# Kernel optimization log

Hardware: AMD Instinct MI355X
Metric: run time of the kernel (lower is better)

Reference implementation:

```python
import jax, jax.numpy as jnp
import numpy as np

TAU = 0.5
EPS = 1e-12  # torch F.normalize default eps


def _l2norm(x):
    n = jnp.sqrt(jnp.sum(x * x, axis=1, keepdims=True))
    return x / jnp.maximum(n, EPS)


def _semi_loss(z1, z2, tau):
    z1n = _l2norm(z1)
    z2n = _l2norm(z2)
    refl = jnp.exp(jnp.matmul(z1n, z1n.T) / tau)      # [N, N]
    between = jnp.exp(jnp.matmul(z1n, z2n.T) / tau)   # [N, N]
    num = jnp.diagonal(between)
    den = refl.sum(axis=1) + between.sum(axis=1) - jnp.diagonal(refl)
    return -jnp.mean(jnp.log(num / den))


def setup_inputs() -> dict:
    key = jax.random.key(0)
    k1, k2 = jax.random.split(key)
    N, D = 8192, 256
    H_1 = jax.random.normal(k1, (N, D), dtype=jnp.float32)
    H_2 = jax.random.normal(k2, (N, D), dtype=jnp.float32)
    return {"H_1": H_1, "H_2": H_2}


def reference(H_1, H_2):
    l1 = _semi_loss(H_1, H_2, TAU)
    l2 = _semi_loss(H_2, H_1, TAU)
    return (l1 + l2) * 0.5
```

## Files before the change

kernel.cpp:

```cpp
#include <hip/hip_runtime.h>
#include <hip/hip_bf16.h>
#include <math.h>

#define NROW 8192
#define DDIM 256
#define BM 128
#define BN 128
#define BK 128
#define NT_SYM 2080
#define NT_FULL 4096

typedef __attribute__((ext_vector_type(4))) float f32x4;
typedef __attribute__((address_space(3))) unsigned int lds_u32;
typedef const __attribute__((address_space(1))) unsigned int glb_u32;

template <int CTRL>
static __device__ inline float dpp_ror_add(float v) {
    int s = __float_as_int(v);
    int r = __builtin_amdgcn_update_dpp(0, s, CTRL, 0xF, 0xF, true);
    return v + __int_as_float(r);
}
static __device__ inline float row16_sum(float v) {
    v = dpp_ror_add<0x121>(v);
    v = dpp_ror_add<0x122>(v);
    v = dpp_ror_add<0x124>(v);
    v = dpp_ror_add<0x128>(v);
    return v;
}

static __device__ inline unsigned int pack_fp8x4(float a, float b, float c, float d) {
    int p = __builtin_amdgcn_cvt_pk_fp8_f32(a, b, 0, false);
    p = __builtin_amdgcn_cvt_pk_fp8_f32(c, d, p, true);
    return (unsigned int)p;
}

__global__ __launch_bounds__(256) void normalize_kernel(
        const float* __restrict__ h1, const float* __restrict__ h2,
        unsigned char* __restrict__ z1b, unsigned char* __restrict__ z2b,
        float* __restrict__ diag,
        float* __restrict__ rs1, float* __restrict__ rs2,
        float* __restrict__ rbr, float* __restrict__ rbc,
        float* __restrict__ out) {
    int wave = threadIdx.x >> 6;
    int lane = threadIdx.x & 63;
    int row  = blockIdx.x * 4 + wave;
    if (blockIdx.x == 0 && threadIdx.x == 0) out[0] = 0.f;
    const float4* p1 = (const float4*)(h1 + (size_t)row * DDIM);
    const float4* p2 = (const float4*)(h2 + (size_t)row * DDIM);
    float4 a = p1[lane];
    float4 b = p2[lane];
    float s1 = a.x*a.x + a.y*a.y + a.z*a.z + a.w*a.w;
    float s2 = b.x*b.x + b.y*b.y + b.z*b.z + b.w*b.w;
    #pragma unroll
    for (int m = 1; m < 64; m <<= 1) { s1 += __shfl_xor(s1, m); s2 += __shfl_xor(s2, m); }
    float r1 = 1.0f / fmaxf(sqrtf(s1), 1e-12f);
    float r2 = 1.0f / fmaxf(sqrtf(s2), 1e-12f);
    float n1x = a.x*r1, n1y = a.y*r1, n1z = a.z*r1, n1w = a.w*r1;
    float n2x = b.x*r2, n2y = b.y*r2, n2z = b.z*r2, n2w = b.w*r2;
    float dt = n1x*n2x + n1y*n2y + n1z*n2z + n1w*n2w;
    #pragma unroll
    for (int m = 1; m < 64; m <<= 1) dt += __shfl_xor(dt, m);
    if (lane == 0) {
        diag[row] = 2.0f * dt;
        rs1[row] = 0.f; rs2[row] = 0.f; rbr[row] = 0.f; rbc[row] = 0.f;
    }
    const float SC = 1.69864364f;
    ((unsigned int*)(z1b + (size_t)row * DDIM))[lane] =
        pack_fp8x4(n1x*SC, n1y*SC, n1z*SC, n1w*SC);
    ((unsigned int*)(z2b + (size_t)row * DDIM))[lane] =
        pack_fp8x4(n2x*SC, n2y*SC, n2z*SC, n2w*SC);
}

__global__ __launch_bounds__(256, 4) void expsum_kernel(
        const unsigned char* __restrict__ z1, const unsigned char* __restrict__ z2,
        float* __restrict__ rs1, float* __restrict__ rs2,
        float* __restrict__ rbr, float* __restrict__ rbc) {
    int b = blockIdx.x;
    int kind, t;
    if (b < NT_SYM)            { kind = 0; t = b; }
    else if (b < 2 * NT_SYM)   { kind = 1; t = b - NT_SYM; }
    else                       { kind = 2; t = b - 2 * NT_SYM; }

    int by, bx;
    const unsigned char *Ap, *Bp;
    float *rowsum, *colsum;
    if (kind == 2) {
        by = t >> 6; bx = t & 63;
        Ap = z1; Bp = z2; rowsum = rbr; colsum = rbc;
    } else {
        by = (int)((sqrtf(8.0f * (float)t + 1.0f) - 1.0f) * 0.5f);
        while ((by + 1) * (by + 2) / 2 <= t) ++by;
        while (by * (by + 1) / 2 > t) --by;
        bx = t - by * (by + 1) / 2;
        const unsigned char* z = (kind == 0) ? z1 : z2;
        Ap = z; Bp = z;
        rowsum = (kind == 0) ? rs1 : rs2;
        colsum = (bx == by) ? nullptr : rowsum;
    }

    const int rt = by * BM;
    const int ct = bx * BN;

    __shared__ __align__(16) unsigned char lA[BM * BK];
    __shared__ __align__(16) unsigned char lB[BN * BK];

    const int tid  = threadIdx.x;
    const int lane = tid & 63;
    const int wid  = tid >> 6;
    const int wr   = wid >> 1;
    const int wc   = wid & 1;
    const int quad = lane >> 4;
    const int l15  = lane & 15;

    const int srow = lane >> 3;
    const int sgt  = lane & 7;

    f32x4 acc[4][4];
    #pragma unroll
    for (int mi = 0; mi < 4; ++mi)
        #pragma unroll
        for (int ni = 0; ni < 4; ++ni)
            acc[mi][ni] = (f32x4){0.f, 0.f, 0.f, 0.f};

    for (int kt = 0; kt < DDIM; kt += BK) {
        #pragma unroll
        for (int p = 0; p < 4; ++p) {
            int r0 = (p * 4 + wid) * 8;
            int r  = r0 + srow;
            int gg = sgt ^ ((r >> 1) & 7);
            const unsigned char* ga = Ap + (size_t)(rt + r) * DDIM + kt + gg * 16;
            __builtin_amdgcn_global_load_lds((glb_u32*)ga, (lds_u32*)(lA + r0 * BK), 16, 0, 0);
            const unsigned char* gb = Bp + (size_t)(ct + r) * DDIM + kt + gg * 16;
            __builtin_amdgcn_global_load_lds((glb_u32*)gb, (lds_u32*)(lB + r0 * BK), 16, 0, 0);
        }
        __syncthreads();
        #pragma unroll
        for (int ks = 0; ks < 4; ++ks) {
            long af[4], bfr[4];
            const int g    = ks * 2 + (quad >> 1);
            const int half = (quad & 1) * 8;
            #pragma unroll
            for (int mi = 0; mi < 4; ++mi) {
                int r = wr * 64 + mi * 16 + l15;
                int phys = (g ^ ((r >> 1) & 7)) * 16 + half;
                af[mi] = *((const long*)(lA + r * BK + phys));
            }
            #pragma unroll
            for (int ni = 0; ni < 4; ++ni) {
                int c = wc * 64 + ni * 16 + l15;
                int phys = (g ^ ((c >> 1) & 7)) * 16 + half;
                bfr[ni] = *((const long*)(lB + c * BK + phys));
            }
            #pragma unroll
            for (int mi = 0; mi < 4; ++mi)
                #pragma unroll
                for (int ni = 0; ni < 4; ++ni)
                    acc[mi][ni] = __builtin_amdgcn_mfma_f32_16x16x32_fp8_fp8(
                        af[mi], bfr[ni], acc[mi][ni], 0, 0, 0);
        }
        __syncthreads();
    }

    float colpart[4] = {0.f, 0.f, 0.f, 0.f};
    #pragma unroll
    for (int mi = 0; mi < 4; ++mi) {
        #pragma unroll
        for (int r = 0; r < 4; ++r) {
            float rp = 0.f;
            #pragma unroll
            for (int ni = 0; ni < 4; ++ni) {
                float e = exp2f(acc[mi][ni][r]);
                rp += e;
                colpart[ni] += e;
            }
            rp = row16_sum(rp);
            if (l15 == 0) {
                int grow = rt + wr * 64 + mi * 16 + quad * 4 + r;
                atomicAdd(&rowsum[grow], rp);
            }
        }
    }
    if (colsum) {
        #pragma unroll
        for (int ni = 0; ni < 4; ++ni) {
            float cp = colpart[ni];
            cp += __shfl_xor(cp, 16);
            cp += __shfl_xor(cp, 32);
            if (lane < 16) {
                int gcol = ct + wc * 64 + ni * 16 + l15;
                atomicAdd(&colsum[gcol], cp);
            }
        }
    }
}

__global__ __launch_bounds__(256) void finalize_kernel(
        const float* __restrict__ rs1, const float* __restrict__ rs2,
        const float* __restrict__ rbr, const float* __restrict__ rbc,
        const float* __restrict__ diag, float* __restrict__ out) {
    __shared__ float s4[4];
    const float E2 = 7.38905609893065f;
    int i = blockIdx.x * 256 + threadIdx.x;
    float den1 = rs1[i] + rbr[i] - E2;
    float den2 = rs2[i] + rbc[i] - E2;
    float v = 0.5f * (logf(den1) + logf(den2)) - diag[i];
    #pragma unroll
    for (int m = 1; m < 64; m <<= 1) v += __shfl_xor(v, m);
    if ((threadIdx.x & 63) == 0) s4[threadIdx.x >> 6] = v;
    __syncthreads();
    if (threadIdx.x == 0) {
        float t = (s4[0] + s4[1] + s4[2] + s4[3]) * (1.0f / (float)NROW);
        atomicAdd(out, t);
    }
}

extern "C" void kernel_launch(void* const* d_in, const int* in_sizes, int n_in,
                              void* d_out, int out_size, void* d_ws, size_t ws_size,
                              hipStream_t stream) {
    const float* h1 = (const float*)d_in[0];
    const float* h2 = (const float*)d_in[1];
    float* out = (float*)d_out;

    char* ws = (char*)d_ws;
    unsigned char* z1b = (unsigned char*)ws;
    unsigned char* z2b = (unsigned char*)(ws + (size_t)NROW * DDIM);
    float* sums = (float*)(ws + (size_t)2 * NROW * DDIM);
    float* rs1  = sums;
    float* rs2  = sums + NROW;
    float* rbr  = sums + 2 * NROW;
    float* rbc  = sums + 3 * NROW;
    float* diag = sums + 4 * NROW;

    normalize_kernel<<<NROW / 4, 256, 0, stream>>>(h1, h2, z1b, z2b, diag,
                                                   rs1, rs2, rbr, rbc, out);

    expsum_kernel<<<2 * NT_SYM + NT_FULL, 256, 0, stream>>>(z1b, z2b, rs1, rs2, rbr, rbc);

    finalize_kernel<<<NROW / 256, 256, 0, stream>>>(rs1, rs2, rbr, rbc, diag, out);
}
```

Before: 169.1 us.

## Use 16x16x128 scaled FP8 MFMA with reworked LDS swizzle and wider fragment loads

Replaces four K-steps of the 16x16x32 FP8 MFMA with one gfx950 scaled MFMA (16x16x128 f8f6f4) per tile pair, using unity scales (0x7F). Operand fragments are now loaded as two 16-byte LDS reads per lane instead of 8-byte reads, and the swizzle is changed from (r>>1)&7 to r&7 to match the new access pattern. This is meant to cut MFMA issue count and LDS instruction count in the inner loop. The larger i32x8 fragments raise register pressure, so launch bounds drop from 4 to 3 blocks per CU, and correctness depends on the lane-to-K mapping matching the new instruction's operand layout.

```diff
diff --git a/kernel.cpp b/kernel.cpp
--- a/kernel.cpp
+++ b/kernel.cpp
@@ -11,6 +11,8 @@
 #define NT_FULL 4096
 
 typedef __attribute__((ext_vector_type(4))) float f32x4;
+typedef __attribute__((ext_vector_type(4))) int   i32x4;
+typedef __attribute__((ext_vector_type(8))) int   i32x8;
 typedef __attribute__((address_space(3))) unsigned int lds_u32;
 typedef const __attribute__((address_space(1))) unsigned int glb_u32;
 
@@ -71,7 +73,7 @@
         pack_fp8x4(n2x*SC, n2y*SC, n2z*SC, n2w*SC);
 }
 
-__global__ __launch_bounds__(256, 4) void expsum_kernel(
+__global__ __launch_bounds__(256, 3) void expsum_kernel(
         const unsigned char* __restrict__ z1, const unsigned char* __restrict__ z2,
         float* __restrict__ rs1, float* __restrict__ rs2,
         float* __restrict__ rbr, float* __restrict__ rbc) {
@@ -114,6 +116,13 @@
 
     const int srow = lane >> 3;
     const int sgt  = lane & 7;
+    const int gg   = sgt ^ srow;
+
+    const int s7 = l15 & 7;
+    const unsigned char* aLo = lA + (wr * 64 + l15) * BK + (((quad << 1)    ) ^ s7) * 16;
+    const unsigned char* aHi = lA + (wr * 64 + l15) * BK + (((quad << 1) | 1) ^ s7) * 16;
+    const unsigned char* bLo = lB + (wc * 64 + l15) * BK + (((quad << 1)    ) ^ s7) * 16;
+    const unsigned char* bHi = lB + (wc * 64 + l15) * BK + (((quad << 1) | 1) ^ s7) * 16;
 
     f32x4 acc[4][4];
     #pragma unroll
@@ -126,38 +135,35 @@
         #pragma unroll
         for (int p = 0; p < 4; ++p) {
             int r0 = (p * 4 + wid) * 8;
-            int r  = r0 + srow;
-            int gg = sgt ^ ((r >> 1) & 7);
-            const unsigned char* ga = Ap + (size_t)(rt + r) * DDIM + kt + gg * 16;
+            const unsigned char* ga = Ap + (size_t)(rt + r0 + srow) * DDIM + kt + gg * 16;
             __builtin_amdgcn_global_load_lds((glb_u32*)ga, (lds_u32*)(lA + r0 * BK), 16, 0, 0);
-            const unsigned char* gb = Bp + (size_t)(ct + r) * DDIM + kt + gg * 16;
+            const unsigned char* gb = Bp + (size_t)(ct + r0 + srow) * DDIM + kt + gg * 16;
             __builtin_amdgcn_global_load_lds((glb_u32*)gb, (lds_u32*)(lB + r0 * BK), 16, 0, 0);
         }
         __syncthreads();
-        #pragma unroll
-        for (int ks = 0; ks < 4; ++ks) {
-            long af[4], bfr[4];
-            const int g    = ks * 2 + (quad >> 1);
-            const int half = (quad & 1) * 8;
+
+        i32x8 af[4], bfr[4];
+        #pragma unroll
+        for (int mi = 0; mi < 4; ++mi) {
+            i32x4 lo = *((const i32x4*)(aLo + mi * 16 * BK));
+            i32x4 hi = *((const i32x4*)(aHi + mi * 16 * BK));
+            af[mi] = __builtin_shufflevector(lo, hi, 0, 1, 2, 3, 4, 5, 6, 7);
+        }
+        #pragma unroll
+        for (int ni = 0; ni < 4; ++ni) {
+            i32x4 lo = *((const i32x4*)(bLo + ni * 16 * BK));
+            i32x4 hi = *((const i32x4*)(bHi + ni * 16 * BK));
+            bfr[ni] = __builtin_shufflevector(lo, hi, 0, 1, 2, 3, 4, 5, 6, 7);
+        }
+        #pragma unroll
+        for (int mi = 0; mi < 4; ++mi)
             #pragma unroll
-            for (int mi = 0; mi < 4; ++mi) {
-                int r = wr * 64 + mi * 16 + l15;
-                int phys = (g ^ ((r >> 1) & 7)) * 16 + half;
-                af[mi] = *((const long*)(lA + r * BK + phys));
-            }
-            #pragma unroll
-            for (int ni = 0; ni < 4; ++ni) {
-                int c = wc * 64 + ni * 16 + l15;
-                int phys = (g ^ ((c >> 1) & 7)) * 16 + half;
-                bfr[ni] = *((const long*)(lB + c * BK + phys));
-            }
-            #pragma unroll
-            for (int mi = 0; mi < 4; ++mi)
-                #pragma unroll
-                for (int ni = 0; ni < 4; ++ni)
-                    acc[mi][ni] = __builtin_amdgcn_mfma_f32_16x16x32_fp8_fp8(
-                        af[mi], bfr[ni], acc[mi][ni], 0, 0, 0);
-        }
+            for (int ni = 0; ni < 4; ++ni)
+                acc[mi][ni] = __builtin_amdgcn_mfma_scale_f32_16x16x128_f8f6f4(
+                    af[mi], bfr[ni], acc[mi][ni],
+                    0, 0,
+                    0, 0x7F7F7F7F,
+                    0, 0x7F7F7F7F);
         __syncthreads();
     }
 
```

New measurement: 173.3 us. 2.5% more time.

## Pre-swizzle fp8 operands into MFMA fragment order for contiguous LDS loads

Applied to the files above, without the earlier changes.

The normalize kernel now writes the fp8 normalized rows in a fragment-major layout, grouped in 16-row blocks, that matches the MFMA 16x16x32 operand layout. The GEMM kernel can then stage tiles with fully contiguous global_load_lds copies and read each lane's operands with a single 16-byte LDS load covering two MFMA k-steps, with no XOR swizzle arithmetic. This is meant to cut address computation and the number of LDS read instructions. The output zeroing also moves from the normalize kernel to a hipMemsetAsync, which adds an extra stream operation. LDS bank-conflict behaviour changes with the new layout and is not verified.

```diff
diff --git a/kernel.cpp b/kernel.cpp
--- a/kernel.cpp
+++ b/kernel.cpp
@@ -6,13 +6,16 @@
 #define DDIM 256
 #define BM 128
 #define BN 128
-#define BK 128
 #define NT_SYM 2080
 #define NT_FULL 4096
+#define NBLOCKS (2 * NT_SYM + NT_FULL)
 
 typedef __attribute__((ext_vector_type(4))) float f32x4;
+typedef __attribute__((ext_vector_type(4))) int   i32x4;
 typedef __attribute__((address_space(3))) unsigned int lds_u32;
 typedef const __attribute__((address_space(1))) unsigned int glb_u32;
+
+union frag_cv { i32x4 v; long l[2]; };
 
 template <int CTRL>
 static __device__ inline float dpp_ror_add(float v) {
@@ -36,15 +39,13 @@
 
 __global__ __launch_bounds__(256) void normalize_kernel(
         const float* __restrict__ h1, const float* __restrict__ h2,
-        unsigned char* __restrict__ z1b, unsigned char* __restrict__ z2b,
+        unsigned int* __restrict__ z1b, unsigned int* __restrict__ z2b,
         float* __restrict__ diag,
         float* __restrict__ rs1, float* __restrict__ rs2,
-        float* __restrict__ rbr, float* __restrict__ rbc,
-        float* __restrict__ out) {
+        float* __restrict__ rbr, float* __restrict__ rbc) {
     int wave = threadIdx.x >> 6;
     int lane = threadIdx.x & 63;
     int row  = blockIdx.x * 4 + wave;
-    if (blockIdx.x == 0 && threadIdx.x == 0) out[0] = 0.f;
     const float4* p1 = (const float4*)(h1 + (size_t)row * DDIM);
     const float4* p2 = (const float4*)(h2 + (size_t)row * DDIM);
     float4 a = p1[lane];
@@ -64,11 +65,15 @@
         diag[row] = 2.0f * dt;
         rs1[row] = 0.f; rs2[row] = 0.f; rbr[row] = 0.f; rbc[row] = 0.f;
     }
+    int t    = lane >> 4;
+    int u    = (lane >> 3) & 1;
+    int quad = (lane >> 1) & 3;
+    int wbit = lane & 1;
+    int g    = row >> 4, rr = row & 15;
+    int pw   = g * 1024 + t * 256 + quad * 64 + rr * 4 + u * 2 + wbit;
     const float SC = 1.69864364f;
-    ((unsigned int*)(z1b + (size_t)row * DDIM))[lane] =
-        pack_fp8x4(n1x*SC, n1y*SC, n1z*SC, n1w*SC);
-    ((unsigned int*)(z2b + (size_t)row * DDIM))[lane] =
-        pack_fp8x4(n2x*SC, n2y*SC, n2z*SC, n2w*SC);
+    z1b[pw] = pack_fp8x4(n1x*SC, n1y*SC, n1z*SC, n1w*SC);
+    z2b[pw] = pack_fp8x4(n2x*SC, n2y*SC, n2z*SC, n2w*SC);
 }
 
 __global__ __launch_bounds__(256, 4) void expsum_kernel(
@@ -76,33 +81,30 @@
         float* __restrict__ rs1, float* __restrict__ rs2,
         float* __restrict__ rbr, float* __restrict__ rbc) {
     int b = blockIdx.x;
-    int kind, t;
-    if (b < NT_SYM)            { kind = 0; t = b; }
-    else if (b < 2 * NT_SYM)   { kind = 1; t = b - NT_SYM; }
-    else                       { kind = 2; t = b - 2 * NT_SYM; }
+    int kind, t0;
+    if (b < NT_SYM)            { kind = 0; t0 = b; }
+    else if (b < 2 * NT_SYM)   { kind = 1; t0 = b - NT_SYM; }
+    else                       { kind = 2; t0 = b - 2 * NT_SYM; }
 
     int by, bx;
     const unsigned char *Ap, *Bp;
     float *rowsum, *colsum;
     if (kind == 2) {
-        by = t >> 6; bx = t & 63;
+        by = t0 >> 6; bx = t0 & 63;
         Ap = z1; Bp = z2; rowsum = rbr; colsum = rbc;
     } else {
-        by = (int)((sqrtf(8.0f * (float)t + 1.0f) - 1.0f) * 0.5f);
-        while ((by + 1) * (by + 2) / 2 <= t) ++by;
-        while (by * (by + 1) / 2 > t) --by;
-        bx = t - by * (by + 1) / 2;
+        by = (int)((sqrtf(8.0f * (float)t0 + 1.0f) - 1.0f) * 0.5f);
+        while ((by + 1) * (by + 2) / 2 <= t0) ++by;
+        while (by * (by + 1) / 2 > t0) --by;
+        bx = t0 - by * (by + 1) / 2;
         const unsigned char* z = (kind == 0) ? z1 : z2;
         Ap = z; Bp = z;
         rowsum = (kind == 0) ? rs1 : rs2;
         colsum = (bx == by) ? nullptr : rowsum;
     }
 
-    const int rt = by * BM;
-    const int ct = bx * BN;
-
-    __shared__ __align__(16) unsigned char lA[BM * BK];
-    __shared__ __align__(16) unsigned char lB[BN * BK];
+    __shared__ __align__(16) unsigned char lA[BM * 128];
+    __shared__ __align__(16) unsigned char lB[BN * 128];
 
     const int tid  = threadIdx.x;
     const int lane = tid & 63;
@@ -112,9 +114,6 @@
     const int quad = lane >> 4;
     const int l15  = lane & 15;
 
-    const int srow = lane >> 3;
-    const int sgt  = lane & 7;
-
     f32x4 acc[4][4];
     #pragma unroll
     for (int mi = 0; mi < 4; ++mi)
@@ -122,44 +121,45 @@
         for (int ni = 0; ni < 4; ++ni)
             acc[mi][ni] = (f32x4){0.f, 0.f, 0.f, 0.f};
 
-    for (int kt = 0; kt < DDIM; kt += BK) {
-        #pragma unroll
-        for (int p = 0; p < 4; ++p) {
-            int r0 = (p * 4 + wid) * 8;
-            int r  = r0 + srow;
-            int gg = sgt ^ ((r >> 1) & 7);
-            const unsigned char* ga = Ap + (size_t)(rt + r) * DDIM + kt + gg * 16;
-            __builtin_amdgcn_global_load_lds((glb_u32*)ga, (lds_u32*)(lA + r0 * BK), 16, 0, 0);
-            const unsigned char* gb = Bp + (size_t)(ct + r) * DDIM + kt + gg * 16;
-            __builtin_amdgcn_global_load_lds((glb_u32*)gb, (lds_u32*)(lB + r0 * BK), 16, 0, 0);
+    for (int kt = 0; kt < 2; ++kt) {
+        #pragma unroll
+        for (int i = 0; i < 4; ++i) {
+            int idx = i * 4 + wid;
+            int tt = idx >> 3, s = idx & 7;
+            const unsigned char* ga = Ap + (((size_t)(by * 8 + s)) << 12)
+                                         + (size_t)(kt * 2 + tt) * 1024 + lane * 16;
+            __builtin_amdgcn_global_load_lds((glb_u32*)ga,
+                                             (lds_u32*)(lA + idx * 1024), 16, 0, 0);
+            const unsigned char* gb = Bp + (((size_t)(bx * 8 + s)) << 12)
+                                         + (size_t)(kt * 2 + tt) * 1024 + lane * 16;
+            __builtin_amdgcn_global_load_lds((glb_u32*)gb,
+                                             (lds_u32*)(lB + idx * 1024), 16, 0, 0);
         }
         __syncthreads();
         #pragma unroll
-        for (int ks = 0; ks < 4; ++ks) {
-            long af[4], bfr[4];
-            const int g    = ks * 2 + (quad >> 1);
-            const int half = (quad & 1) * 8;
-            #pragma unroll
-            for (int mi = 0; mi < 4; ++mi) {
-                int r = wr * 64 + mi * 16 + l15;
-                int phys = (g ^ ((r >> 1) & 7)) * 16 + half;
-                af[mi] = *((const long*)(lA + r * BK + phys));
-            }
-            #pragma unroll
-            for (int ni = 0; ni < 4; ++ni) {
-                int c = wc * 64 + ni * 16 + l15;
-                int phys = (g ^ ((c >> 1) & 7)) * 16 + half;
-                bfr[ni] = *((const long*)(lB + c * BK + phys));
-            }
+        for (int tt = 0; tt < 2; ++tt) {
+            frag_cv va[4], vb[4];
+            #pragma unroll
+            for (int mi = 0; mi < 4; ++mi)
+                va[mi].v = *((const i32x4*)(lA + (tt * 8 + wr * 4 + mi) * 1024 + lane * 16));
+            #pragma unroll
+            for (int ni = 0; ni < 4; ++ni)
+                vb[ni].v = *((const i32x4*)(lB + (tt * 8 + wc * 4 + ni) * 1024 + lane * 16));
             #pragma unroll
             for (int mi = 0; mi < 4; ++mi)
                 #pragma unroll
-                for (int ni = 0; ni < 4; ++ni)
+                for (int ni = 0; ni < 4; ++ni) {
                     acc[mi][ni] = __builtin_amdgcn_mfma_f32_16x16x32_fp8_fp8(
-                        af[mi], bfr[ni], acc[mi][ni], 0, 0, 0);
+                        va[mi].l[0], vb[ni].l[0], acc[mi][ni], 0, 0, 0);
+                    acc[mi][ni] = __builtin_amdgcn_mfma_f32_16x16x32_fp8_fp8(
+                        va[mi].l[1], vb[ni].l[1], acc[mi][ni], 0, 0, 0);
+                }
         }
         __syncthreads();
     }
+
+    const int rt = by * BM;
+    const int ct = bx * BN;
 
     float colpart[4] = {0.f, 0.f, 0.f, 0.f};
     #pragma unroll
@@ -231,10 +231,13 @@
     float* rbc  = sums + 3 * NROW;
     float* diag = sums + 4 * NROW;
 
-    normalize_kernel<<<NROW / 4, 256, 0, stream>>>(h1, h2, z1b, z2b, diag,
-                                                   rs1, rs2, rbr, rbc, out);
-
-    expsum_kernel<<<2 * NT_SYM + NT_FULL, 256, 0, stream>>>(z1b, z2b, rs1, rs2, rbr, rbc);
+    hipMemsetAsync(out, 0, sizeof(float), stream);
+
+    normalize_kernel<<<NROW / 4, 256, 0, stream>>>(h1, h2,
+                                                   (unsigned int*)z1b, (unsigned int*)z2b,
+                                                   diag, rs1, rs2, rbr, rbc);
+
+    expsum_kernel<<<NBLOCKS, 256, 0, stream>>>(z1b, z2b, rs1, rs2, rbr, rbc);
 
     finalize_kernel<<<NROW / 256, 256, 0, stream>>>(rs1, rs2, rbr, rbc, diag, out);
 }
```

Measured after the change: 174.6 us. 3.2% more time.
